# Kernel tuning notes

Measured on AMD Instinct MI355X. Metric: run time of the kernel, lower is better.

The kernel has to match this reference:

```python
import jax, jax.numpy as jnp
import numpy as np

N_HEADS = 12
B, S, D = 2, 2048, 768
NEG = -1e9


def setup_inputs() -> dict:
    key = jax.random.key(0)
    ks = jax.random.split(key, 7)
    scale = 1.0 / np.sqrt(D)
    Q = jax.random.normal(ks[0], (B, S, D), jnp.float32)
    K = jax.random.normal(ks[1], (B, S, D), jnp.float32)
    V = jax.random.normal(ks[2], (B, S, D), jnp.float32)
    # causal mask, broadcastable over batch and heads; 0 entries are masked out
    mask = jnp.tril(jnp.ones((S, S), jnp.int32))[None, None, :, :]
    Wq = jax.random.normal(ks[3], (D, D), jnp.float32) * scale
    Wk = jax.random.normal(ks[4], (D, D), jnp.float32) * scale
    Wv = jax.random.normal(ks[5], (D, D), jnp.float32) * scale
    Wo = jax.random.normal(ks[6], (D, D), jnp.float32) * scale
    return {"Q": Q, "K": K, "V": V, "mask": mask,
            "Wq": Wq, "Wk": Wk, "Wv": Wv, "Wo": Wo}


def reference(Q, K, V, mask, Wq, Wk, Wv, Wo):
    b, s, d = Q.shape
    h = N_HEADS
    dk = d // h
    # projections (torch nn.Linear: x @ W.T), split heads -> (b, h, s, dk)
    q = (Q @ Wq.T).reshape(b, s, h, dk).transpose(0, 2, 1, 3)
    k = (K @ Wk.T).reshape(b, s, h, dk).transpose(0, 2, 1, 3)
    v = (V @ Wv.T).reshape(b, s, h, dk).transpose(0, 2, 1, 3)
    scores = jnp.einsum('bhqd,bhkd->bhqk', q, k) / jnp.sqrt(jnp.asarray(dk, q.dtype))
    scores = jnp.where(mask == 0, jnp.asarray(NEG, scores.dtype), scores)
    attn = jax.nn.softmax(scores, axis=-1)  # dropout p=0.0 -> identity
    ctx = jnp.einsum('bhqk,bhkd->bhqd', attn, v)
    ctx = ctx.transpose(0, 2, 1, 3).reshape(b, s, d)
    return ctx @ Wo.T
```

## Files before the change

kernel.cpp:

```cpp
#include <hip/hip_runtime.h>
#include <math.h>

#define NH     12
#define BB     2
#define SEQ    2048
#define DMODEL 768
#define DK     64

typedef __attribute__((ext_vector_type(8))) short short8;
typedef __attribute__((ext_vector_type(4))) short short4v;
typedef __attribute__((ext_vector_type(4))) float floatx4;

__device__ __forceinline__ unsigned short f2bf(float x) {
    unsigned u = __builtin_bit_cast(unsigned, x);
    u = (u + 0x7fffu + ((u >> 16) & 1u)) >> 16;
    return (unsigned short)u;
}
__device__ __forceinline__ unsigned short f2bf_fast(float x) {
    unsigned u = __builtin_bit_cast(unsigned, x);
    return (unsigned short)((u + 0x8000u) >> 16);
}
__device__ __forceinline__ float bf2f(unsigned short h) {
    unsigned u = ((unsigned)h) << 16;
    return __builtin_bit_cast(float, u);
}

__device__ __forceinline__ void gld_lds16(const ushort* gptr, ushort* lptr) {
    __builtin_amdgcn_global_load_lds(
        (const __attribute__((address_space(1))) unsigned int*)(const void*)gptr,
        (__attribute__((address_space(3))) unsigned int*)(void*)lptr,
        16, 0, 0);
}

__device__ __forceinline__ short4v shfl8(short4v v, int src) {
    int2 t = __builtin_bit_cast(int2, v);
    t.x = __shfl(t.x, src);
    t.y = __shfl(t.y, src);
    return __builtin_bit_cast(short4v, t);
}

#define SI (BB * SEQ * DMODEL)
#define SW (DMODEL * DMODEL)

#define P1_BLOCKS 1024
#define NPART     8
#define ITPP      216
#define SHPP      (P1_BLOCKS / NPART)

__global__ __launch_bounds__(256) void cast_w(
    const float* __restrict__ Wq, const float* __restrict__ Wk,
    const float* __restrict__ Wv, const float* __restrict__ Wo,
    ushort* oWq, ushort* oWk, ushort* oWv, ushort* oWo, int* counter) {
    if (blockIdx.x == 0 && threadIdx.x < NPART) counter[threadIdx.x] = SHPP;
    long i = (long)(blockIdx.x * 256 + threadIdx.x) * 4;
    const float* src; ushort* dst; long off;
    if      (i < 1L * SW) { src = Wq; dst = oWq; off = i; }
    else if (i < 2L * SW) { src = Wk; dst = oWk; off = i - 1L * SW; }
    else if (i < 3L * SW) { src = Wv; dst = oWv; off = i - 2L * SW; }
    else                  { src = Wo; dst = oWo; off = i - 3L * SW; }
    float4 v = *(const float4*)(src + off);
    ushort4 o;
    o.x = f2bf(v.x); o.y = f2bf(v.y); o.z = f2bf(v.z); o.w = f2bf(v.w);
    *(ushort4*)(dst + off) = o;
}

template<int MODE, bool AF32, int TM>
__device__ __forceinline__ void gemm_body(ushort* __restrict__ Sbase,
                                          const void* __restrict__ Av,
                                          const ushort* __restrict__ W,
                                          float* __restrict__ outF,
                                          ushort* __restrict__ outH,
                                          float scale) {
    constexpr int ATS = TM * 32;
    constexpr int BST = ATS + 128 * 32;
    constexpr int MI  = TM / 32;
    constexpr int AIT = TM / 64;
    constexpr int NWG = (TM == 128) ? 192 : 384;

    const int lin = blockIdx.y * 6 + blockIdx.x;
    const int swz = (lin & 7) * (NWG / 8) + (lin >> 3);
    const int n0 = (swz % 6) * 128;
    const int m0 = (swz / 6) * TM;

    const int tid  = threadIdx.x;
    const int lane = tid & 63;
    const int wv   = tid >> 6;
    const int l15  = lane & 15;
    const int quad = lane >> 4;
    const int wm = (wv >> 1) * (TM / 2);
    const int wn = (wv & 1) * 64;

    const int srow = tid >> 2;
    const int sch  = tid & 3;
    const int schx = sch ^ ((srow >> 1) & 3);
    const int sw2  = (l15 >> 1) & 3;

    const ushort* Ab = (const ushort*)Av;
    const float*  Af = (const float*)Av;

    floatx4 acc[MI][4];
    #pragma unroll
    for (int i = 0; i < MI; ++i)
        #pragma unroll
        for (int j = 0; j < 4; ++j) acc[i][j] = (floatx4)0.f;

    float4 ar0[2], ar1[2];
    #pragma unroll
    for (int it = 0; it < AIT; ++it) {
        const int r = srow + it * 64;
        if (AF32) {
            const float* p = Af + (size_t)(m0 + r) * DMODEL + schx * 8;
            ar0[it] = *(const float4*)p;
            ar1[it] = *(const float4*)(p + 4);
        } else {
            gld_lds16(Ab + (size_t)(m0 + r) * DMODEL + schx * 8, Sbase + r * 32 + sch * 8);
        }
    }
    #pragma unroll
    for (int it = 0; it < 2; ++it) {
        const int r = srow + it * 64;
        gld_lds16(W + (size_t)(n0 + r) * DMODEL + schx * 8, Sbase + ATS + r * 32 + sch * 8);
    }
    if (AF32) {
        #pragma unroll
        for (int it = 0; it < AIT; ++it) {
            const int r = srow + it * 64;
            short8 s8;
            s8[0] = (short)f2bf_fast(ar0[it].x); s8[1] = (short)f2bf_fast(ar0[it].y);
            s8[2] = (short)f2bf_fast(ar0[it].z); s8[3] = (short)f2bf_fast(ar0[it].w);
            s8[4] = (short)f2bf_fast(ar1[it].x); s8[5] = (short)f2bf_fast(ar1[it].y);
            s8[6] = (short)f2bf_fast(ar1[it].z); s8[7] = (short)f2bf_fast(ar1[it].w);
            *(short8*)(Sbase + r * 32 + sch * 8) = s8;
        }
    }

    const int NS = DMODEL / 32;
    for (int t = 0; t < NS; ++t) {
        __syncthreads();
        const int bi = (t + 1) & 1;
        ushort* SbufN = Sbase + bi * BST;
        if (t + 1 < NS) {
            const int k0 = (t + 1) * 32;
            #pragma unroll
            for (int it = 0; it < AIT; ++it) {
                const int r = srow + it * 64;
                if (AF32) {
                    const float* p = Af + (size_t)(m0 + r) * DMODEL + k0 + schx * 8;
                    ar0[it] = *(const float4*)p;
                    ar1[it] = *(const float4*)(p + 4);
                } else {
                    gld_lds16(Ab + (size_t)(m0 + r) * DMODEL + k0 + schx * 8, SbufN + r * 32 + sch * 8);
                }
            }
            #pragma unroll
            for (int it = 0; it < 2; ++it) {
                const int r = srow + it * 64;
                gld_lds16(W + (size_t)(n0 + r) * DMODEL + k0 + schx * 8, SbufN + ATS + r * 32 + sch * 8);
            }
        }
        const ushort* As  = Sbase + (t & 1) * BST;
        const ushort* Ws2 = As + ATS;
        short8 af[MI], bf[4];
        #pragma unroll
        for (int mi = 0; mi < MI; ++mi)
            af[mi] = *(const short8*)&As[(wm + mi * 16 + l15) * 32 + ((quad ^ sw2) * 8)];
        #pragma unroll
        for (int ni = 0; ni < 4; ++ni)
            bf[ni] = *(const short8*)&Ws2[(wn + ni * 16 + l15) * 32 + ((quad ^ sw2) * 8)];
        #pragma unroll
        for (int mi = 0; mi < MI; ++mi)
            #pragma unroll
            for (int ni = 0; ni < 4; ++ni) {
                if (MODE == 2)
                    acc[mi][ni] = __builtin_amdgcn_mfma_f32_16x16x32_bf16(bf[ni], af[mi], acc[mi][ni], 0, 0, 0);
                else
                    acc[mi][ni] = __builtin_amdgcn_mfma_f32_16x16x32_bf16(af[mi], bf[ni], acc[mi][ni], 0, 0, 0);
            }
        if (AF32 && t + 1 < NS) {
            #pragma unroll
            for (int it = 0; it < AIT; ++it) {
                const int r = srow + it * 64;
                short8 s8;
                s8[0] = (short)f2bf_fast(ar0[it].x); s8[1] = (short)f2bf_fast(ar0[it].y);
                s8[2] = (short)f2bf_fast(ar0[it].z); s8[3] = (short)f2bf_fast(ar0[it].w);
                s8[4] = (short)f2bf_fast(ar1[it].x); s8[5] = (short)f2bf_fast(ar1[it].y);
                s8[6] = (short)f2bf_fast(ar1[it].z); s8[7] = (short)f2bf_fast(ar1[it].w);
                *(short8*)(SbufN + r * 32 + sch * 8) = s8;
            }
        }
    }

    #pragma unroll
    for (int mi = 0; mi < MI; ++mi)
        #pragma unroll
        for (int ni = 0; ni < 4; ++ni)
            #pragma unroll
            for (int r = 0; r < 4; ++r) {
                const float v = acc[mi][ni][r] * scale;
                if (MODE == 2) {
                    const int m = m0 + wm + mi * 16 + l15;
                    const int n = n0 + wn + ni * 16 + quad * 4 + r;
                    const int b = m >> 11, s = m & (SEQ - 1);
                    const int h = n >> 6,  dk = n & 63;
                    outH[(((size_t)b * NH + h) * DK + dk) * SEQ + s] = f2bf(v);
                } else {
                    const int m = m0 + wm + mi * 16 + quad * 4 + r;
                    const int n = n0 + wn + ni * 16 + l15;
                    if (MODE == 0) {
                        outF[(size_t)m * DMODEL + n] = v;
                    } else {
                        const int b = m >> 11, s = m & (SEQ - 1);
                        const int h = n >> 6,  dk = n & 63;
                        outH[(((size_t)b * NH + h) * SEQ + s) * DK + dk] = f2bf(v);
                    }
                }
            }
}

#define QSCALE (0.125f * 1.44269504088896f)

__global__ __launch_bounds__(256) void gemm_qkv(
    const float* Q, const float* K, const float* V,
    const ushort* Wqb, const ushort* Wkb, const ushort* Wvb,
    ushort* qh, ushort* kh, ushort* vhT) {
    __shared__ __align__(16) ushort S[2 * (128 * 32 + 128 * 32)];
    const int z = blockIdx.z;
    if (z == 0)      gemm_body<1, true, 128>(S, Q, Wqb, nullptr, qh,  QSCALE);
    else if (z == 1) gemm_body<1, true, 128>(S, K, Wkb, nullptr, kh,  1.0f);
    else             gemm_body<2, true, 128>(S, V, Wvb, nullptr, vhT, 1.0f);
}

__global__ __launch_bounds__(256) void gemm_out(const ushort* A, const ushort* W, float* out) {
    __shared__ __align__(16) ushort S[2 * (64 * 32 + 128 * 32)];
    gemm_body<0, false, 64>(S, A, W, out, nullptr, 1.0f);
}

#define NIT   (24 * 72)
#define MBIAS -20.0f
__device__ const int d_offs[17] = {0,1,2,4,6,9,12,16,20,25,30,36,42,49,56,64,72};

__global__ __launch_bounds__(256, 4) void flash_p1(const ushort* __restrict__ qh,
                                                   const ushort* __restrict__ kh,
                                                   const ushort* __restrict__ vhT,
                                                   ushort* __restrict__ ctx,
                                                   ushort* __restrict__ Opart,
                                                   float* __restrict__ lpart,
                                                   int* __restrict__ counter) {
    const int tid  = threadIdx.x;
    const int lane = tid & 63;
    const int wv   = tid >> 6;
    const int l15  = lane & 15;
    const int quad = lane >> 4;

    __shared__ __align__(16) ushort KV[2][2][64 * 64];
    __shared__ int wshare;

    const int srow = tid >> 3;
    const int sch  = tid & 7;
    const int schx = sch ^ (srow & 7);
    const int swq  = l15 & 7;

    const int srcA = l15 + 32 * (quad & 1);
    const int srcB = srcA + 16;
    const bool hiq = (quad >> 1) != 0;

    const int colc[2] = { ((quad ^ swq) * 8), (((4 + quad) ^ swq) * 8) };

    const int part   = blockIdx.x & (NPART - 1);
    const int itbase = part * ITPP;
    int lidx = blockIdx.x >> 3;
    for (;;) {
        if (lidx >= ITPP) break;
        if (tid == 0) wshare = atomicAdd(counter + part, 1);
        const int item = itbase + (ITPP - 1 - lidx);
        const int bh = item / 72;
        const int r72 = item - bh * 72;
        int Q = 0;
        #pragma unroll
        for (int q = 0; q < 16; ++q) if (r72 >= d_offs[q + 1]) Q = q + 1;
        const int s  = r72 - d_offs[Q];
        const int ns = (Q >> 1) + 1;
        const int b  = bh / NH, h = bh % NH;
        const int qbase = Q * 128;
        const int k_lo = 4 * s;
        const int k_hi = min(4 * s + 3, 2 * Q + 1);

        const ushort* kbase = kh  + (size_t)bh * SEQ * DK;
        const ushort* vbase = vhT + (size_t)bh * DK * SEQ;

        short8 qf[2][2];
        #pragma unroll
        for (int qs = 0; qs < 2; ++qs) {
            const ushort* qp = qh + ((size_t)bh * SEQ + qbase + wv * 32 + qs * 16 + l15) * DK;
            qf[qs][0] = *(const short8*)(qp + quad * 8);
            qf[qs][1] = *(const short8*)(qp + 32 + quad * 8);
        }

        {
            const int k0 = k_lo * 64;
            gld_lds16(kbase + (size_t)(k0 + srow) * DK + schx * 8,        &KV[0][0][srow * 64 + sch * 8]);
            gld_lds16(kbase + (size_t)(k0 + srow + 32) * DK + schx * 8,   &KV[0][0][(srow + 32) * 64 + sch * 8]);
            gld_lds16(vbase + (size_t)srow * SEQ + k0 + schx * 8,         &KV[0][1][srow * 64 + sch * 8]);
            gld_lds16(vbase + (size_t)(srow + 32) * SEQ + k0 + schx * 8,  &KV[0][1][(srow + 32) * 64 + sch * 8]);
        }

        float l_s[2] = {0.f, 0.f};
        floatx4 o_acc[2][4];
        #pragma unroll
        for (int qs = 0; qs < 2; ++qs)
            #pragma unroll
            for (int d = 0; d < 4; ++d) o_acc[qs][d] = (floatx4)0.f;

        for (int kt = k_lo; kt <= k_hi; ++kt) {
            __syncthreads();
            if (kt < k_hi) {
                const int k0 = (kt + 1) * 64;
                const int bi = (kt + 1 - k_lo) & 1;
                gld_lds16(kbase + (size_t)(k0 + srow) * DK + schx * 8,        &KV[bi][0][srow * 64 + sch * 8]);
                gld_lds16(kbase + (size_t)(k0 + srow + 32) * DK + schx * 8,   &KV[bi][0][(srow + 32) * 64 + sch * 8]);
                gld_lds16(vbase + (size_t)srow * SEQ + k0 + schx * 8,         &KV[bi][1][srow * 64 + sch * 8]);
                gld_lds16(vbase + (size_t)(srow + 32) * SEQ + k0 + schx * 8,  &KV[bi][1][(srow + 32) * 64 + sch * 8]);
            }
            const int cb = (kt - k_lo) & 1;
            const ushort* Ks  = KV[cb][0];
            const ushort* Vts = KV[cb][1];
            const bool diag = (kt >= 2 * Q);

            floatx4 s_acc[2][4];
            #pragma unroll
            for (int qs = 0; qs < 2; ++qs)
                #pragma unroll
                for (int nt = 0; nt < 4; ++nt) s_acc[qs][nt] = (floatx4)(MBIAS);
            #pragma unroll
            for (int kc = 0; kc < 2; ++kc)
                #pragma unroll
                for (int nt = 0; nt < 4; ++nt) {
                    short8 kf = *(const short8*)&Ks[(nt * 16 + l15) * 64 + colc[kc]];
                    s_acc[0][nt] = __builtin_amdgcn_mfma_f32_16x16x32_bf16(kf, qf[0][kc], s_acc[0][nt], 0, 0, 0);
                    s_acc[1][nt] = __builtin_amdgcn_mfma_f32_16x16x32_bf16(kf, qf[1][kc], s_acc[1][nt], 0, 0, 0);
                }

            if (diag) {
                #pragma unroll
                for (int qs = 0; qs < 2; ++qs) {
                    const int qg = qbase + wv * 32 + qs * 16 + l15;
                    #pragma unroll
                    for (int nt = 0; nt < 4; ++nt)
                        #pragma unroll
                        for (int rr = 0; rr < 4; ++rr)
                            if (kt * 64 + nt * 16 + quad * 4 + rr > qg) s_acc[qs][nt][rr] = -1.0e30f;
                }
            }

            short4v packed[2][4];
            #pragma unroll
            for (int qs = 0; qs < 2; ++qs) {
                float lp0 = 0.f, lp1 = 0.f, lp2 = 0.f, lp3 = 0.f;
                #pragma unroll
                for (int nt = 0; nt < 4; ++nt)
                    #pragma unroll
                    for (int rr = 0; rr < 4; ++rr) {
                        const float pe = exp2f(s_acc[qs][nt][rr]);
                        if      (rr == 0) lp0 += pe;
                        else if (rr == 1) lp1 += pe;
                        else if (rr == 2) lp2 += pe;
                        else              lp3 += pe;
                        packed[qs][nt][rr] = (short)f2bf_fast(pe);
                    }
                l_s[qs] += (lp0 + lp1) + (lp2 + lp3);
            }

            #pragma unroll
            for (int kc = 0; kc < 2; ++kc) {
                short8 pf[2];
                #pragma unroll
                for (int qs = 0; qs < 2; ++qs) {
                    short4v a0 = shfl8(packed[qs][2 * kc],     srcA);
                    short4v a1 = shfl8(packed[qs][2 * kc + 1], srcA);
                    short4v b0 = shfl8(packed[qs][2 * kc],     srcB);
                    short4v b1 = shfl8(packed[qs][2 * kc + 1], srcB);
                    short4v lo = hiq ? a1 : a0;
                    short4v hi = hiq ? b1 : b0;
                    pf[qs][0] = lo[0]; pf[qs][1] = lo[1]; pf[qs][2] = lo[2]; pf[qs][3] = lo[3];
                    pf[qs][4] = hi[0]; pf[qs][5] = hi[1]; pf[qs][6] = hi[2]; pf[qs][7] = hi[3];
                }
                #pragma unroll
                for (int dkt = 0; dkt < 4; ++dkt) {
                    short8 vf = *(const short8*)&Vts[(dkt * 16 + l15) * 64 + colc[kc]];
                    o_acc[0][dkt] = __builtin_amdgcn_mfma_f32_16x16x32_bf16(pf[0], vf, o_acc[0][dkt], 0, 0, 0);
                    o_acc[1][dkt] = __builtin_amdgcn_mfma_f32_16x16x32_bf16(pf[1], vf, o_acc[1][dkt], 0, 0, 0);
                }
            }
        }

        #pragma unroll
        for (int qs = 0; qs < 2; ++qs) {
            l_s[qs] += __shfl_xor(l_s[qs], 16);
            l_s[qs] += __shfl_xor(l_s[qs], 32);
        }

        if (ns == 1) {
            #pragma unroll
            for (int qs = 0; qs < 2; ++qs)
                #pragma unroll
                for (int rr = 0; rr < 4; ++rr) {
                    const float lr = __shfl(l_s[qs], quad * 20 + rr);
                    const float inv = 1.f / lr;
                    const int sg = qbase + wv * 32 + qs * 16 + quad * 4 + rr;
                    #pragma unroll
                    for (int dkt = 0; dkt < 4; ++dkt) {
                        const int d = h * DK + dkt * 16 + l15;
                        ctx[((size_t)b * SEQ + sg) * DMODEL + d] = f2bf(o_acc[qs][dkt][rr] * inv);
                    }
                }
        } else {
            const int pid = bh * 70 + (d_offs[Q] - 2) + s;
            ushort* op = Opart + (size_t)pid * (128 * 64);
            #pragma unroll
            for (int qs = 0; qs < 2; ++qs) {
                #pragma unroll
                for (int rr = 0; rr < 4; ++rr) {
                    const int row = wv * 32 + qs * 16 + quad * 4 + rr;
                    #pragma unroll
                    for (int dkt = 0; dkt < 4; ++dkt)
                        op[row * 64 + dkt * 16 + l15] = f2bf(o_acc[qs][dkt][rr]);
                }
                if (quad == 0)
                    lpart[(size_t)pid * 128 + wv * 32 + qs * 16 + l15] = l_s[qs];
            }
        }

        lidx = __builtin_amdgcn_readfirstlane(wshare);
        __syncthreads();
    }
}

__global__ __launch_bounds__(256) void flash_combine(const ushort* __restrict__ Opart,
                                                     const float* __restrict__ lpart,
                                                     ushort* __restrict__ ctx) {
    const int blk = blockIdx.x;
    const int rh  = blk & 3;
    const int Q   = 2 + ((blk >> 2) % 14);
    const int bh  = blk / 56;
    const int ns = (Q >> 1) + 1;
    const int pbase = bh * 70 + (d_offs[Q] - 2);
    const int b = bh / NH, h = bh % NH;
    const int t = threadIdx.x;
    const int row = rh * 32 + (t >> 3);
    const int c0  = (t & 7) * 8;

    float lt = 0.f;
    for (int s2 = 0; s2 < ns; ++s2) lt += lpart[(size_t)(pbase + s2) * 128 + row];
    const float inv = 1.f / lt;

    float acc[8];
    #pragma unroll
    for (int j = 0; j < 8; ++j) acc[j] = 0.f;
    for (int s2 = 0; s2 < ns; ++s2) {
        const ushort* op = Opart + (size_t)(pbase + s2) * (128 * 64) + row * 64 + c0;
        short8 v = *(const short8*)op;
        #pragma unroll
        for (int e = 0; e < 8; ++e) acc[e] += bf2f((unsigned short)v[e]);
    }
    ushort* dst = ctx + ((size_t)b * SEQ + Q * 128 + row) * DMODEL + h * DK + c0;
    short8 o;
    #pragma unroll
    for (int e = 0; e < 8; ++e) o[e] = (short)f2bf(acc[e] * inv);
    *(short8*)dst = o;
}

extern "C" void kernel_launch(void* const* d_in, const int* in_sizes, int n_in,
                              void* d_out, int out_size, void* d_ws, size_t ws_size,
                              hipStream_t stream) {
    const float* Q  = (const float*)d_in[0];
    const float* K  = (const float*)d_in[1];
    const float* V  = (const float*)d_in[2];
    const float* Wq = (const float*)d_in[4];
    const float* Wk = (const float*)d_in[5];
    const float* Wv = (const float*)d_in[6];
    const float* Wo = (const float*)d_in[7];

    char* ws = (char*)d_ws;
    const size_t SZ_IN = (size_t)SI * 2;
    const size_t SZ_W  = (size_t)SW * 2;
    ushort* Wqb   = (ushort*)(ws);
    ushort* Wkb   = (ushort*)(ws + SZ_W);
    ushort* Wvb   = (ushort*)(ws + 2 * SZ_W);
    ushort* Wob   = (ushort*)(ws + 3 * SZ_W);
    ushort* qh    = (ushort*)(ws + 4 * SZ_W);
    ushort* kh    = (ushort*)(ws + 4 * SZ_W + SZ_IN);
    ushort* vhT   = (ushort*)(ws + 4 * SZ_W + 2 * SZ_IN);
    ushort* ctx   = (ushort*)(ws + 4 * SZ_W + 3 * SZ_IN);
    ushort* Opart = (ushort*)(ws + 4 * SZ_W + 4 * SZ_IN);
    float*  lpart = (float*) (ws + 4 * SZ_W + 4 * SZ_IN + (size_t)1680 * 8192 * 2);
    int*    ctr   = (int*)   (ws + 4 * SZ_W + 4 * SZ_IN + (size_t)1680 * 8192 * 2
                                 + (size_t)1680 * 128 * 4);

    dim3 blk(256);
    cast_w<<<dim3(4 * SW / 1024), blk, 0, stream>>>(Wq, Wk, Wv, Wo,
                                                    Wqb, Wkb, Wvb, Wob, ctr);
    gemm_qkv<<<dim3(6, 32, 3), blk, 0, stream>>>(Q, K, V, Wqb, Wkb, Wvb, qh, kh, vhT);
    flash_p1<<<dim3(P1_BLOCKS), blk, 0, stream>>>(qh, kh, vhT, ctx, Opart, lpart, ctr);
    flash_combine<<<dim3(24 * 14 * 4), blk, 0, stream>>>(Opart, lpart, ctx);
    gemm_out<<<dim3(6, 64), blk, 0, stream>>>(ctx, Wob, (float*)d_out);
}
```

Measured before the change: 204.5 us.

## Process two K-steps per barrier in projection GEMMs with four LDS buffers

The projection GEMM main loop now handles two 32-wide K slices per iteration. It uses four LDS stage buffers, prefetching the next two slices while computing the current two. This halves the number of __syncthreads barriers and deepens the load pipeline. In exchange it doubles the LDS footprint of both GEMM kernels, to 64 KB for the QKV GEMM, which can lower occupancy, and it holds twice as many fp32 staging registers.

```diff
diff --git a/kernel.cpp b/kernel.cpp
--- a/kernel.cpp
+++ b/kernel.cpp
@@ -64,6 +64,76 @@
     *(ushort4*)(dst + off) = o;
 }
 
+template<bool AF32, int TM>
+__device__ __forceinline__ void g_stage_issue(const float* __restrict__ Af,
+                                              const ushort* __restrict__ Ab,
+                                              const ushort* __restrict__ W,
+                                              ushort* __restrict__ Sb,
+                                              int m0, int n0, int k0,
+                                              int srow, int sch, int schx,
+                                              float4* ar0, float4* ar1) {
+    constexpr int AIT = TM / 64;
+    constexpr int ATS = TM * 32;
+    #pragma unroll
+    for (int it = 0; it < AIT; ++it) {
+        const int r = srow + it * 64;
+        if constexpr (AF32) {
+            const float* p = Af + (size_t)(m0 + r) * DMODEL + k0 + schx * 8;
+            ar0[it] = *(const float4*)p;
+            ar1[it] = *(const float4*)(p + 4);
+        } else {
+            gld_lds16(Ab + (size_t)(m0 + r) * DMODEL + k0 + schx * 8, Sb + r * 32 + sch * 8);
+        }
+    }
+    #pragma unroll
+    for (int it = 0; it < 2; ++it) {
+        const int r = srow + it * 64;
+        gld_lds16(W + (size_t)(n0 + r) * DMODEL + k0 + schx * 8, Sb + ATS + r * 32 + sch * 8);
+    }
+}
+
+template<int TM>
+__device__ __forceinline__ void g_writeA(ushort* __restrict__ Sb, int srow, int sch,
+                                         const float4* ar0, const float4* ar1) {
+    constexpr int AIT = TM / 64;
+    #pragma unroll
+    for (int it = 0; it < AIT; ++it) {
+        const int r = srow + it * 64;
+        short8 s8;
+        s8[0] = (short)f2bf_fast(ar0[it].x); s8[1] = (short)f2bf_fast(ar0[it].y);
+        s8[2] = (short)f2bf_fast(ar0[it].z); s8[3] = (short)f2bf_fast(ar0[it].w);
+        s8[4] = (short)f2bf_fast(ar1[it].x); s8[5] = (short)f2bf_fast(ar1[it].y);
+        s8[6] = (short)f2bf_fast(ar1[it].z); s8[7] = (short)f2bf_fast(ar1[it].w);
+        *(short8*)(Sb + r * 32 + sch * 8) = s8;
+    }
+}
+
+template<int MODE, int TM>
+__device__ __forceinline__ void g_compute(const ushort* __restrict__ Sb,
+                                          floatx4 (&acc)[TM / 32][4],
+                                          int wm, int wn, int l15, int quad, int sw2) {
+    constexpr int MI  = TM / 32;
+    constexpr int ATS = TM * 32;
+    const ushort* As  = Sb;
+    const ushort* Ws2 = Sb + ATS;
+    short8 af[MI], bf[4];
+    #pragma unroll
+    for (int mi = 0; mi < MI; ++mi)
+        af[mi] = *(const short8*)&As[(wm + mi * 16 + l15) * 32 + ((quad ^ sw2) * 8)];
+    #pragma unroll
+    for (int ni = 0; ni < 4; ++ni)
+        bf[ni] = *(const short8*)&Ws2[(wn + ni * 16 + l15) * 32 + ((quad ^ sw2) * 8)];
+    #pragma unroll
+    for (int mi = 0; mi < MI; ++mi)
+        #pragma unroll
+        for (int ni = 0; ni < 4; ++ni) {
+            if (MODE == 2)
+                acc[mi][ni] = __builtin_amdgcn_mfma_f32_16x16x32_bf16(bf[ni], af[mi], acc[mi][ni], 0, 0, 0);
+            else
+                acc[mi][ni] = __builtin_amdgcn_mfma_f32_16x16x32_bf16(af[mi], bf[ni], acc[mi][ni], 0, 0, 0);
+        }
+}
+
 template<int MODE, bool AF32, int TM>
 __device__ __forceinline__ void gemm_body(ushort* __restrict__ Sbase,
                                           const void* __restrict__ Av,
@@ -104,88 +174,30 @@
         #pragma unroll
         for (int j = 0; j < 4; ++j) acc[i][j] = (floatx4)0.f;
 
-    float4 ar0[2], ar1[2];
-    #pragma unroll
-    for (int it = 0; it < AIT; ++it) {
-        const int r = srow + it * 64;
-        if (AF32) {
-            const float* p = Af + (size_t)(m0 + r) * DMODEL + schx * 8;
-            ar0[it] = *(const float4*)p;
-            ar1[it] = *(const float4*)(p + 4);
-        } else {
-            gld_lds16(Ab + (size_t)(m0 + r) * DMODEL + schx * 8, Sbase + r * 32 + sch * 8);
-        }
-    }
-    #pragma unroll
-    for (int it = 0; it < 2; ++it) {
-        const int r = srow + it * 64;
-        gld_lds16(W + (size_t)(n0 + r) * DMODEL + schx * 8, Sbase + ATS + r * 32 + sch * 8);
-    }
-    if (AF32) {
-        #pragma unroll
-        for (int it = 0; it < AIT; ++it) {
-            const int r = srow + it * 64;
-            short8 s8;
-            s8[0] = (short)f2bf_fast(ar0[it].x); s8[1] = (short)f2bf_fast(ar0[it].y);
-            s8[2] = (short)f2bf_fast(ar0[it].z); s8[3] = (short)f2bf_fast(ar0[it].w);
-            s8[4] = (short)f2bf_fast(ar1[it].x); s8[5] = (short)f2bf_fast(ar1[it].y);
-            s8[6] = (short)f2bf_fast(ar1[it].z); s8[7] = (short)f2bf_fast(ar1[it].w);
-            *(short8*)(Sbase + r * 32 + sch * 8) = s8;
-        }
+    float4 ar0[2][AIT], ar1[2][AIT];
+
+    g_stage_issue<AF32, TM>(Af, Ab, W, Sbase,           m0, n0, 0,  srow, sch, schx, ar0[0], ar1[0]);
+    g_stage_issue<AF32, TM>(Af, Ab, W, Sbase + BST,     m0, n0, 32, srow, sch, schx, ar0[1], ar1[1]);
+    if constexpr (AF32) {
+        g_writeA<TM>(Sbase,       srow, sch, ar0[0], ar1[0]);
+        g_writeA<TM>(Sbase + BST, srow, sch, ar0[1], ar1[1]);
     }
 
     const int NS = DMODEL / 32;
-    for (int t = 0; t < NS; ++t) {
+    for (int t = 0; t < NS; t += 2) {
         __syncthreads();
-        const int bi = (t + 1) & 1;
-        ushort* SbufN = Sbase + bi * BST;
-        if (t + 1 < NS) {
-            const int k0 = (t + 1) * 32;
-            #pragma unroll
-            for (int it = 0; it < AIT; ++it) {
-                const int r = srow + it * 64;
-                if (AF32) {
-                    const float* p = Af + (size_t)(m0 + r) * DMODEL + k0 + schx * 8;
-                    ar0[it] = *(const float4*)p;
-                    ar1[it] = *(const float4*)(p + 4);
-                } else {
-                    gld_lds16(Ab + (size_t)(m0 + r) * DMODEL + k0 + schx * 8, SbufN + r * 32 + sch * 8);
-                }
-            }
-            #pragma unroll
-            for (int it = 0; it < 2; ++it) {
-                const int r = srow + it * 64;
-                gld_lds16(W + (size_t)(n0 + r) * DMODEL + k0 + schx * 8, SbufN + ATS + r * 32 + sch * 8);
-            }
-        }
-        const ushort* As  = Sbase + (t & 1) * BST;
-        const ushort* Ws2 = As + ATS;
-        short8 af[MI], bf[4];
-        #pragma unroll
-        for (int mi = 0; mi < MI; ++mi)
-            af[mi] = *(const short8*)&As[(wm + mi * 16 + l15) * 32 + ((quad ^ sw2) * 8)];
-        #pragma unroll
-        for (int ni = 0; ni < 4; ++ni)
-            bf[ni] = *(const short8*)&Ws2[(wn + ni * 16 + l15) * 32 + ((quad ^ sw2) * 8)];
-        #pragma unroll
-        for (int mi = 0; mi < MI; ++mi)
-            #pragma unroll
-            for (int ni = 0; ni < 4; ++ni) {
-                if (MODE == 2)
-                    acc[mi][ni] = __builtin_amdgcn_mfma_f32_16x16x32_bf16(bf[ni], af[mi], acc[mi][ni], 0, 0, 0);
-                else
-                    acc[mi][ni] = __builtin_amdgcn_mfma_f32_16x16x32_bf16(af[mi], bf[ni], acc[mi][ni], 0, 0, 0);
-            }
-        if (AF32 && t + 1 < NS) {
-            #pragma unroll
-            for (int it = 0; it < AIT; ++it) {
-                const int r = srow + it * 64;
-                short8 s8;
-                s8[0] = (short)f2bf_fast(ar0[it].x); s8[1] = (short)f2bf_fast(ar0[it].y);
-                s8[2] = (short)f2bf_fast(ar0[it].z); s8[3] = (short)f2bf_fast(ar0[it].w);
-                s8[4] = (short)f2bf_fast(ar1[it].x); s8[5] = (short)f2bf_fast(ar1[it].y);
-                s8[6] = (short)f2bf_fast(ar1[it].z); s8[7] = (short)f2bf_fast(ar1[it].w);
-                *(short8*)(SbufN + r * 32 + sch * 8) = s8;
+        ushort* SbA = Sbase + ((t + 2) & 3) * BST;
+        ushort* SbB = Sbase + ((t + 3) & 3) * BST;
+        if (t + 2 < NS) {
+            g_stage_issue<AF32, TM>(Af, Ab, W, SbA, m0, n0, (t + 2) * 32, srow, sch, schx, ar0[0], ar1[0]);
+            g_stage_issue<AF32, TM>(Af, Ab, W, SbB, m0, n0, (t + 3) * 32, srow, sch, schx, ar0[1], ar1[1]);
+        }
+        g_compute<MODE, TM>(Sbase + (t & 3) * BST,       acc, wm, wn, l15, quad, sw2);
+        g_compute<MODE, TM>(Sbase + ((t + 1) & 3) * BST, acc, wm, wn, l15, quad, sw2);
+        if constexpr (AF32) {
+            if (t + 2 < NS) {
+                g_writeA<TM>(SbA, srow, sch, ar0[0], ar1[0]);
+                g_writeA<TM>(SbB, srow, sch, ar0[1], ar1[1]);
             }
         }
     }
@@ -223,7 +235,7 @@
     const float* Q, const float* K, const float* V,
     const ushort* Wqb, const ushort* Wkb, const ushort* Wvb,
     ushort* qh, ushort* kh, ushort* vhT) {
-    __shared__ __align__(16) ushort S[2 * (128 * 32 + 128 * 32)];
+    __shared__ __align__(16) ushort S[4 * (128 * 32 + 128 * 32)];
     const int z = blockIdx.z;
     if (z == 0)      gemm_body<1, true, 128>(S, Q, Wqb, nullptr, qh,  QSCALE);
     else if (z == 1) gemm_body<1, true, 128>(S, K, Wkb, nullptr, kh,  1.0f);
@@ -231,7 +243,7 @@
 }
 
 __global__ __launch_bounds__(256) void gemm_out(const ushort* A, const ushort* W, float* out) {
-    __shared__ __align__(16) ushort S[2 * (64 * 32 + 128 * 32)];
+    __shared__ __align__(16) ushort S[4 * (64 * 32 + 128 * 32)];
     gemm_body<0, false, 64>(S, A, W, out, nullptr, 1.0f);
 }
 
```

After: 214.3 us. 1.05x slower.
